# Kernel optimization log

Hardware: AMD Instinct MI355X
Metric: run time of the kernel (lower is better)

The kernel has to match this reference:

```python
import jax, jax.numpy as jnp
import numpy as np

N = 100000      # nodes
E = 1250000     # edges
DIN = 128       # in_channels
H = 64          # hidden
DOUT = 40       # out_channels


def setup_inputs() -> dict:
    key = jax.random.key(0)
    k0, k1, k2, k3 = jax.random.split(key, 4)
    x = jax.random.normal(k0, (N, DIN), dtype=jnp.float32)
    edge_index = jax.random.randint(k1, (2, E), 0, N, dtype=jnp.int32)
    # glorot-style init for the GCNConv linear layers
    W1 = jax.random.normal(k2, (DIN, H), dtype=jnp.float32) * np.float32(1.0 / np.sqrt(DIN))
    b1 = jnp.zeros((H,), dtype=jnp.float32)
    W2 = jax.random.normal(k3, (H, DOUT), dtype=jnp.float32) * np.float32(1.0 / np.sqrt(H))
    b2 = jnp.zeros((DOUT,), dtype=jnp.float32)
    return {"x": x, "W1": W1, "b1": b1, "W2": W2, "b2": b2, "edge_index": edge_index}


def reference(x, W1, b1, W2, b2, edge_index):
    # GCN normalization with added self-loops (PyG GCNConv default):
    # norm_e = deg(dst)^-1/2 * deg(src)^-1/2
    loop = jnp.arange(N, dtype=edge_index.dtype)
    src = jnp.concatenate([edge_index[0], loop])
    dst = jnp.concatenate([edge_index[1], loop])
    deg = jax.ops.segment_sum(jnp.ones(src.shape[0], x.dtype), dst, num_segments=N)
    dinv = jax.lax.rsqrt(deg)  # deg >= 1 thanks to self-loops
    norm = dinv[src] * dinv[dst]  # [E+N]

    def gcn_conv(h, W, b):
        h = h @ W                                     # [N, d_out] linear (no bias)
        msg = h[src] * norm[:, None]                  # gather + normalize
        return jax.ops.segment_sum(msg, dst, num_segments=N) + b  # scatter-add + bias

    h = jax.nn.relu(gcn_conv(x, W1, b1))  # dropout p=0.0 -> identity
    return gcn_conv(h, W2, b2)
```

## Files before the change

### kernel.cpp

```cpp
#include <hip/hip_runtime.h>
#include <hip/hip_fp16.h>

#define NN   100000
#define EE   1250000
#define DIN  128
#define HID  64
#define DOUT 40

#define BN   512
#define NB   196
#define CH   4096
#define SEG  8192
#define S_BLKS 306
#define G_BLKS 1563

typedef _Float16 v8h __attribute__((ext_vector_type(8)));
typedef float    v4f __attribute__((ext_vector_type(4)));

__device__ __forceinline__ void acc8(const float4& v, float4& lo, float4& hi) {
    const __half2* hp = (const __half2*)&v;
    float2 f0 = __half22float2(hp[0]), f1 = __half22float2(hp[1]);
    float2 f2 = __half22float2(hp[2]), f3 = __half22float2(hp[3]);
    lo.x += f0.x; lo.y += f0.y; lo.z += f1.x; lo.w += f1.y;
    hi.x += f2.x; hi.y += f2.y; hi.z += f3.x; hi.w += f3.y;
}

__global__ __launch_bounds__(256) void k_wprep(const float* __restrict__ W1,
                                               const float* __restrict__ W2,
                                               __half* __restrict__ w1frag,
                                               __half* __restrict__ w2frag,
                                               int* __restrict__ bucket_fill) {
    int t = threadIdx.x;
    if (blockIdx.x == 5 && t < NB) bucket_fill[t] = 0;
    int e = blockIdx.x * 256 + t;
    if (e < 1024) {
        int ct = e >> 8, ki = (e >> 6) & 3, l = e & 63;
        int q = l >> 4, n = l & 15;
        v8h o;
        #pragma unroll
        for (int j = 0; j < 8; ++j)
            o[j] = (_Float16)W1[(ki * 32 + q * 8 + j) * 64 + ct * 16 + n];
        ((v8h*)w1frag)[e] = o;
    } else {
        int e2 = e - 1024;
        if (e2 < 384) {
            int ct = e2 >> 7, ki = (e2 >> 6) & 1, l = e2 & 63;
            int q = l >> 4, n = l & 15;
            int col = ct * 16 + n;
            v8h o;
            #pragma unroll
            for (int j = 0; j < 8; ++j)
                o[j] = (col < DOUT) ? (_Float16)W2[(ki * 32 + q * 8 + j) * DOUT + col]
                                    : (_Float16)0.0f;
            ((v8h*)w2frag)[e2] = o;
        }
    }
}

__global__ __launch_bounds__(256) void k_fat(const int* __restrict__ src,
                                             const int* __restrict__ dst,
                                             int* __restrict__ bucket_fill,
                                             int* __restrict__ ebuf,
                                             const float* __restrict__ x,
                                             const __half* __restrict__ w1frag,
                                             __half* __restrict__ xw1h) {
    __shared__ int smem[4096];
    int t = threadIdx.x;
    if (blockIdx.x < S_BLKS) {
        int* hist  = smem;
        int* gbase = smem + 256;
        int* rcur  = smem + 512;
        for (int i = t; i < NB; i += 256) { hist[i] = 0; rcur[i] = 0; }
        __syncthreads();
        int e0 = blockIdx.x * CH;
        int ep[16], eb[16];
        #pragma unroll
        for (int j = 0; j < 16; ++j) {
            int e = e0 + j * 256 + t;
            bool valid = (e < EE);
            if (valid) {
                int dd_ = dst[e];
                ep[j] = (src[e] << 9) | (dd_ & 511);
                eb[j] = dd_ >> 9;
                atomicAdd(&hist[eb[j]], 1);
            } else {
                ep[j] = 0; eb[j] = -1;
            }
        }
        __syncthreads();
        for (int i = t; i < NB; i += 256)
            gbase[i] = atomicAdd(&bucket_fill[i], hist[i]);
        __syncthreads();
        #pragma unroll
        for (int j = 0; j < 16; ++j) {
            if (eb[j] >= 0) {
                int r = atomicAdd(&rcur[eb[j]], 1);
                ebuf[eb[j] * SEG + gbase[eb[j]] + r] = ep[j];
            }
        }
    } else {
        float4* sb4 = (float4*)smem;
        const float4* wf = (const float4*)w1frag;
        #pragma unroll
        for (int i = 0; i < 4; ++i) sb4[t + i * 256] = wf[t + i * 256];
        __syncthreads();
        const v8h* sbh = (const v8h*)sb4;
        int wv = t >> 6, l = t & 63;
        int q = l >> 4, n = l & 15;
        int row0 = (blockIdx.x - S_BLKS) * 64 + wv * 16;
        int m = row0 + n;
        bool mv = (m < NN);
        const float* xr = x + (size_t)(mv ? m : 0) * DIN + q * 8;
        v8h afrag[4];
        #pragma unroll
        for (int ki = 0; ki < 4; ++ki) {
            float4 u0 = mv ? ((const float4*)(xr + ki * 32))[0] : make_float4(0.f,0.f,0.f,0.f);
            float4 u1 = mv ? ((const float4*)(xr + ki * 32))[1] : make_float4(0.f,0.f,0.f,0.f);
            v8h a;
            a[0] = (_Float16)u0.x; a[1] = (_Float16)u0.y;
            a[2] = (_Float16)u0.z; a[3] = (_Float16)u0.w;
            a[4] = (_Float16)u1.x; a[5] = (_Float16)u1.y;
            a[6] = (_Float16)u1.z; a[7] = (_Float16)u1.w;
            afrag[ki] = a;
        }
        v4f acc[4];
        #pragma unroll
        for (int ct = 0; ct < 4; ++ct) acc[ct] = (v4f){0.f, 0.f, 0.f, 0.f};
        #pragma unroll
        for (int ct = 0; ct < 4; ++ct) {
            #pragma unroll
            for (int ki = 0; ki < 4; ++ki)
                acc[ct] = __builtin_amdgcn_mfma_f32_16x16x32_f16(
                    afrag[ki], sbh[(ct * 4 + ki) * 64 + l], acc[ct], 0, 0, 0);
        }
        _Float16* outh = (_Float16*)xw1h;
        #pragma unroll
        for (int r = 0; r < 4; ++r) {
            int rr = row0 + q * 4 + r;
            if (rr < NN) {
                #pragma unroll
                for (int ct = 0; ct < 4; ++ct)
                    outh[(size_t)rr * HID + ct * 16 + n] = (_Float16)acc[ct][r];
            }
        }
    }
}

__global__ __launch_bounds__(256) void kB_csr(const int* __restrict__ ebuf,
                                              const int* __restrict__ bucket_fill,
                                              int* __restrict__ pofs,
                                              float* __restrict__ dinv,
                                              int* __restrict__ esrc,
                                              __half* __restrict__ xw1h) {
    __shared__ int lcnt[BN], sA[BN], sB[BN], lcur[BN];
    int t = threadIdx.x;
    int b = blockIdx.x;
    int eb0 = b * SEG;
    int ecnt = bucket_fill[b];
    lcnt[t] = 0; lcnt[t + 256] = 0;
    __syncthreads();
    for (int j = t; j < ecnt; j += 256)
        atomicAdd(&lcnt[ebuf[eb0 + j] & 511], 1);
    __syncthreads();
    sA[t] = lcnt[t]; sA[t + 256] = lcnt[t + 256];
    __syncthreads();
    int* s = sA; int* d = sB;
    for (int off = 1; off < BN; off <<= 1) {
        d[t] = s[t] + ((t >= off) ? s[t - off] : 0);
        int i2 = t + 256;
        d[i2] = s[i2] + ((i2 >= off) ? s[i2 - off] : 0);
        __syncthreads();
        int* tmp = s; s = d; d = tmp;
    }
    int base_node = b * BN;
    #pragma unroll
    for (int k = 0; k < 2; ++k) {
        int i = t + k * 256;
        int excl = s[i] - lcnt[i];
        lcur[i] = excl;
        int node = base_node + i;
        if (node < NN) {
            pofs[node] = ((eb0 + excl) << 10) | lcnt[i];
            dinv[node] = rsqrtf((float)lcnt[i] + 1.0f);
        }
    }
    __syncthreads();
    for (int j = t; j < ecnt; j += 256) {
        int p = ebuf[eb0 + j];
        int r = atomicAdd(&lcur[p & 511], 1);
        esrc[eb0 + r] = p >> 9;
    }
    float4* xr4 = (float4*)xw1h;
    for (int i = t; i < BN * 8; i += 256) {
        int li = i >> 3;
        int node = base_node + li;
        if (node < NN) {
            float di = rsqrtf((float)lcnt[li] + 1.0f);
            float4 v = xr4[(size_t)node * 8 + (i & 7)];
            __half2* h = (__half2*)&v;
            #pragma unroll
            for (int u = 0; u < 4; ++u) {
                float2 f = __half22float2(h[u]);
                h[u] = __floats2half2_rn(f.x * di, f.y * di);
            }
            xr4[(size_t)node * 8 + (i & 7)] = v;
        }
    }
}

__global__ __launch_bounds__(256) void k_fuse(const __half* __restrict__ xw1h,
                                              const float* __restrict__ dinv,
                                              const int* __restrict__ pofs,
                                              const int* __restrict__ esrc,
                                              const float* __restrict__ b1,
                                              const __half* __restrict__ w2frag,
                                              __half* __restrict__ hw2p) {
    __shared__ float4 sb4[384];
    __shared__ __half sh[64 * 72];
    __shared__ float sb1[64];
    int t = threadIdx.x;
    const float4* wf = (const float4*)w2frag;
    if (t < 192) { sb4[t] = wf[t]; sb4[t + 192] = wf[t + 192]; }
    if (t >= 192) sb1[t - 192] = b1[t - 192];
    int d0 = blockIdx.x * 64;
    int g = t >> 3, q = t & 7;
    const float4* tab4 = (const float4*)xw1h;
    #pragma unroll
    for (int sub = 0; sub < 2; ++sub) {
        int d = d0 + g * 2 + sub;
        if (d < NN) {
            float4 lo = make_float4(0.f, 0.f, 0.f, 0.f);
            float4 hi = make_float4(0.f, 0.f, 0.f, 0.f);
            acc8(tab4[(size_t)d * 8 + q], lo, hi);
            int p = pofs[d];
            int j = p >> 10, je = j + (p & 1023);
            for (; j + 7 < je; j += 8) {
                int ss[8];
                #pragma unroll
                for (int u = 0; u < 8; ++u) ss[u] = esrc[j + u];
                float4 vv[8];
                #pragma unroll
                for (int u = 0; u < 8; ++u) vv[u] = tab4[(size_t)ss[u] * 8 + q];
                #pragma unroll
                for (int u = 0; u < 8; ++u) acc8(vv[u], lo, hi);
            }
            for (; j + 3 < je; j += 4) {
                float4 v0 = tab4[(size_t)esrc[j] * 8 + q];
                float4 v1 = tab4[(size_t)esrc[j + 1] * 8 + q];
                float4 v2 = tab4[(size_t)esrc[j + 2] * 8 + q];
                float4 v3 = tab4[(size_t)esrc[j + 3] * 8 + q];
                acc8(v0, lo, hi); acc8(v1, lo, hi);
                acc8(v2, lo, hi); acc8(v3, lo, hi);
            }
            for (; j < je; ++j)
                acc8(tab4[(size_t)esrc[j] * 8 + q], lo, hi);
            float dd = dinv[d];
            float4 st;
            __half2* hp = (__half2*)&st;
            hp[0] = __floats2half2_rn(dd * lo.x, dd * lo.y);
            hp[1] = __floats2half2_rn(dd * lo.z, dd * lo.w);
            hp[2] = __floats2half2_rn(dd * hi.x, dd * hi.y);
            hp[3] = __floats2half2_rn(dd * hi.z, dd * hi.w);
            *(float4*)(sh + (g * 2 + sub) * 72 + q * 8) = st;
        }
    }
    __syncthreads();
    const v8h* sbh = (const v8h*)sb4;
    int wv = t >> 6, l = t & 63;
    int qq = l >> 4, n = l & 15;
    int srow = wv * 16 + n;
    v8h afrag[2];
    #pragma unroll
    for (int ki = 0; ki < 2; ++ki) {
        v8h a = *(const v8h*)(sh + srow * 72 + ki * 32 + qq * 8);
        #pragma unroll
        for (int j = 0; j < 8; ++j) {
            float av = (float)a[j] + sb1[ki * 32 + qq * 8 + j];
            a[j] = (_Float16)fmaxf(av, 0.f);
        }
        afrag[ki] = a;
    }
    v4f acc[3];
    #pragma unroll
    for (int ct = 0; ct < 3; ++ct) acc[ct] = (v4f){0.f, 0.f, 0.f, 0.f};
    #pragma unroll
    for (int ct = 0; ct < 3; ++ct) {
        #pragma unroll
        for (int ki = 0; ki < 2; ++ki)
            acc[ct] = __builtin_amdgcn_mfma_f32_16x16x32_f16(
                afrag[ki], sbh[(ct * 2 + ki) * 64 + l], acc[ct], 0, 0, 0);
    }
    _Float16* outh = (_Float16*)hw2p;
    #pragma unroll
    for (int r = 0; r < 4; ++r) {
        int rr = d0 + wv * 16 + qq * 4 + r;
        if (rr < NN) {
            float di = dinv[rr];
            #pragma unroll
            for (int ct = 0; ct < 3; ++ct)
                outh[(size_t)rr * 64 + ct * 16 + n] = (_Float16)(acc[ct][r] * di);
        }
    }
}

__global__ __launch_bounds__(256) void k_agg2(const __half* __restrict__ hw2p,
                                              const float* __restrict__ dinv,
                                              const int* __restrict__ pofs,
                                              const int* __restrict__ esrc,
                                              const float* __restrict__ b2,
                                              float* __restrict__ out) {
    int t = threadIdx.x;
    int g = t >> 3, q = t & 7;
    int d = blockIdx.x * 32 + g;
    if (d >= NN) return;
    const float4* tab4 = (const float4*)hw2p;
    float4 lo = make_float4(0.f, 0.f, 0.f, 0.f);
    float4 hi = make_float4(0.f, 0.f, 0.f, 0.f);
    acc8(tab4[(size_t)d * 8 + q], lo, hi);
    int p = pofs[d];
    int j = p >> 10, je = j + (p & 1023);
    for (; j + 7 < je; j += 8) {
        int ss[8];
        #pragma unroll
        for (int u = 0; u < 8; ++u) ss[u] = esrc[j + u];
        float4 vv[8];
        #pragma unroll
        for (int u = 0; u < 8; ++u) vv[u] = tab4[(size_t)ss[u] * 8 + q];
        #pragma unroll
        for (int u = 0; u < 8; ++u) acc8(vv[u], lo, hi);
    }
    for (; j + 3 < je; j += 4) {
        float4 v0 = tab4[(size_t)esrc[j] * 8 + q];
        float4 v1 = tab4[(size_t)esrc[j + 1] * 8 + q];
        float4 v2 = tab4[(size_t)esrc[j + 2] * 8 + q];
        float4 v3 = tab4[(size_t)esrc[j + 3] * 8 + q];
        acc8(v0, lo, hi); acc8(v1, lo, hi);
        acc8(v2, lo, hi); acc8(v3, lo, hi);
    }
    for (; j < je; ++j)
        acc8(tab4[(size_t)esrc[j] * 8 + q], lo, hi);
    if (q < 5) {
        float dd = dinv[d];
        const float4* b24 = (const float4*)(b2 + q * 8);
        float4 bl = b24[0], bh = b24[1];
        float* op = out + (size_t)d * DOUT + q * 8;
        ((float4*)op)[0] = make_float4(dd * lo.x + bl.x, dd * lo.y + bl.y,
                                       dd * lo.z + bl.z, dd * lo.w + bl.w);
        ((float4*)op)[1] = make_float4(dd * hi.x + bh.x, dd * hi.y + bh.y,
                                       dd * hi.z + bh.z, dd * hi.w + bh.w);
    }
}

extern "C" void kernel_launch(void* const* d_in, const int* in_sizes, int n_in,
                              void* d_out, int out_size, void* d_ws, size_t ws_size,
                              hipStream_t stream) {
    const float* x  = (const float*)d_in[0];
    const float* W1 = (const float*)d_in[1];
    const float* b1 = (const float*)d_in[2];
    const float* W2 = (const float*)d_in[3];
    const float* b2 = (const float*)d_in[4];
    const int*   ei = (const int*)d_in[5];
    const int* src = ei;
    const int* dst = ei + EE;
    float* out = (float*)d_out;

    float* ws = (float*)d_ws;
    int*    bucket_fill = (int*)ws;
    int*    pofs        = (int*)ws + 256;
    float*  dinv        = ws + 100352;
    int*    ebuf        = (int*)ws + 200704;
    int*    esrc        = (int*)ws + 1806336;
    __half* xw1h        = (__half*)(ws + 3411968);
    __half* hw2p        = (__half*)(ws + 6611968);
    __half* w1frag      = (__half*)(ws + 9811968);
    __half* w2frag      = (__half*)(ws + 9816064);

    k_wprep <<<6, 256, 0, stream>>>(W1, W2, w1frag, w2frag, bucket_fill);
    k_fat   <<<S_BLKS + G_BLKS, 256, 0, stream>>>(src, dst, bucket_fill, ebuf, x, w1frag, xw1h);
    kB_csr  <<<NB, 256, 0, stream>>>(ebuf, bucket_fill, pofs, dinv, esrc, xw1h);
    k_fuse  <<<(NN + 63) / 64, 256, 0, stream>>>(xw1h, dinv, pofs, esrc, b1, w2frag, hw2p);
    k_agg2  <<<(NN + 31) / 32, 256, 0, stream>>>(hw2p, dinv, pofs, esrc, b2, out);
}
```

Baseline: 201.0 us.

## Switch gathers to edge-balanced chunks with shared-memory segmented atomic accumulation

Both aggregation kernels now split the CSR edge range of each 64-node tile evenly across 32 thread groups instead of giving one group per destination node. Each group keeps running sums and flushes them with shared-memory atomics when the destination changes. To support this, the local destination index is packed into the upper bits of esrc. The aim is to remove load imbalance from varying degrees and the tail loops, at the cost of LDS atomics, an extra barrier, and in agg2 idle lanes for q>=5 during the gather.

```diff
diff --git a/kernel.cpp b/kernel.cpp
--- a/kernel.cpp
+++ b/kernel.cpp
@@ -24,6 +24,21 @@
     lo.x += f0.x; lo.y += f0.y; lo.z += f1.x; lo.w += f1.y;
     hi.x += f2.x; hi.y += f2.y; hi.z += f3.x; hi.w += f3.y;
 }
+
+__device__ __forceinline__ void flush8(float* p, const float4& lo, const float4& hi) {
+    atomicAdd(p + 0, lo.x); atomicAdd(p + 1, lo.y);
+    atomicAdd(p + 2, lo.z); atomicAdd(p + 3, lo.w);
+    atomicAdd(p + 4, hi.x); atomicAdd(p + 5, hi.y);
+    atomicAdd(p + 6, hi.z); atomicAdd(p + 7, hi.w);
+}
+
+#define PROC(dl_, v_) { int dl__ = (dl_);                                        \
+    if (dl__ != cur) {                                                           \
+        if (cur >= 0) flush8(&lacc[(cur - dlo) * 72 + q * 8], lo, hi);           \
+        cur = dl__;                                                              \
+        lo = make_float4(0.f,0.f,0.f,0.f); hi = make_float4(0.f,0.f,0.f,0.f);    \
+    }                                                                            \
+    acc8(v_, lo, hi); }
 
 __global__ __launch_bounds__(256) void k_wprep(const float* __restrict__ W1,
                                                const float* __restrict__ W2,
@@ -188,7 +203,7 @@
     for (int j = t; j < ecnt; j += 256) {
         int p = ebuf[eb0 + j];
         int r = atomicAdd(&lcur[p & 511], 1);
-        esrc[eb0 + r] = p >> 9;
+        esrc[eb0 + r] = (p >> 9) | ((p & 511) << 17);
     }
     float4* xr4 = (float4*)xw1h;
     for (int i = t; i < BN * 8; i += 256) {
@@ -215,68 +230,73 @@
                                               const float* __restrict__ b1,
                                               const __half* __restrict__ w2frag,
                                               __half* __restrict__ hw2p) {
+    __shared__ float lacc[64 * 72];
     __shared__ float4 sb4[384];
-    __shared__ __half sh[64 * 72];
     __shared__ float sb1[64];
     int t = threadIdx.x;
     const float4* wf = (const float4*)w2frag;
     if (t < 192) { sb4[t] = wf[t]; sb4[t + 192] = wf[t + 192]; }
     if (t >= 192) sb1[t - 192] = b1[t - 192];
+    for (int i = t; i < 64 * 72; i += 256) lacc[i] = 0.f;
+    __syncthreads();
+
     int d0 = blockIdx.x * 64;
+    int dlo = d0 & 511;
+    int lastd = min(d0 + 63, NN - 1);
+    int pA = pofs[d0], pB = pofs[lastd];
+    int j0 = pA >> 10;
+    int j1 = (pB >> 10) + (pB & 1023);
     int g = t >> 3, q = t & 7;
+    int nchunk = (j1 - j0 + 31) >> 5;
+    int js = j0 + g * nchunk;
+    int je = min(js + nchunk, j1);
     const float4* tab4 = (const float4*)xw1h;
-    #pragma unroll
-    for (int sub = 0; sub < 2; ++sub) {
-        int d = d0 + g * 2 + sub;
-        if (d < NN) {
-            float4 lo = make_float4(0.f, 0.f, 0.f, 0.f);
-            float4 hi = make_float4(0.f, 0.f, 0.f, 0.f);
-            acc8(tab4[(size_t)d * 8 + q], lo, hi);
-            int p = pofs[d];
-            int j = p >> 10, je = j + (p & 1023);
-            for (; j + 7 < je; j += 8) {
-                int ss[8];
-                #pragma unroll
-                for (int u = 0; u < 8; ++u) ss[u] = esrc[j + u];
-                float4 vv[8];
-                #pragma unroll
-                for (int u = 0; u < 8; ++u) vv[u] = tab4[(size_t)ss[u] * 8 + q];
-                #pragma unroll
-                for (int u = 0; u < 8; ++u) acc8(vv[u], lo, hi);
-            }
-            for (; j + 3 < je; j += 4) {
-                float4 v0 = tab4[(size_t)esrc[j] * 8 + q];
-                float4 v1 = tab4[(size_t)esrc[j + 1] * 8 + q];
-                float4 v2 = tab4[(size_t)esrc[j + 2] * 8 + q];
-                float4 v3 = tab4[(size_t)esrc[j + 3] * 8 + q];
-                acc8(v0, lo, hi); acc8(v1, lo, hi);
-                acc8(v2, lo, hi); acc8(v3, lo, hi);
-            }
-            for (; j < je; ++j)
-                acc8(tab4[(size_t)esrc[j] * 8 + q], lo, hi);
-            float dd = dinv[d];
-            float4 st;
-            __half2* hp = (__half2*)&st;
-            hp[0] = __floats2half2_rn(dd * lo.x, dd * lo.y);
-            hp[1] = __floats2half2_rn(dd * lo.z, dd * lo.w);
-            hp[2] = __floats2half2_rn(dd * hi.x, dd * hi.y);
-            hp[3] = __floats2half2_rn(dd * hi.z, dd * hi.w);
-            *(float4*)(sh + (g * 2 + sub) * 72 + q * 8) = st;
-        }
-    }
-    __syncthreads();
+
+    float4 lo = make_float4(0.f,0.f,0.f,0.f), hi = make_float4(0.f,0.f,0.f,0.f);
+    int cur = -1;
+    int j = js;
+    for (; j + 3 < je; j += 4) {
+        int e0 = esrc[j], e1 = esrc[j+1], e2 = esrc[j+2], e3 = esrc[j+3];
+        float4 v0 = tab4[(size_t)(e0 & 0x1FFFF) * 8 + q];
+        float4 v1 = tab4[(size_t)(e1 & 0x1FFFF) * 8 + q];
+        float4 v2 = tab4[(size_t)(e2 & 0x1FFFF) * 8 + q];
+        float4 v3 = tab4[(size_t)(e3 & 0x1FFFF) * 8 + q];
+        PROC(e0 >> 17, v0); PROC(e1 >> 17, v1);
+        PROC(e2 >> 17, v2); PROC(e3 >> 17, v3);
+    }
+    for (; j < je; ++j) {
+        int e = esrc[j];
+        float4 v = tab4[(size_t)(e & 0x1FFFF) * 8 + q];
+        PROC(e >> 17, v);
+    }
+    if (cur >= 0) flush8(&lacc[(cur - dlo) * 72 + q * 8], lo, hi);
+    __syncthreads();
+
     const v8h* sbh = (const v8h*)sb4;
     int wv = t >> 6, l = t & 63;
     int qq = l >> 4, n = l & 15;
     int srow = wv * 16 + n;
+    int node = d0 + srow;
+    bool nv = (node < NN);
+    float dd = nv ? dinv[node] : 0.f;
     v8h afrag[2];
     #pragma unroll
     for (int ki = 0; ki < 2; ++ki) {
-        v8h a = *(const v8h*)(sh + srow * 72 + ki * 32 + qq * 8);
-        #pragma unroll
-        for (int j = 0; j < 8; ++j) {
-            float av = (float)a[j] + sb1[ki * 32 + qq * 8 + j];
-            a[j] = (_Float16)fmaxf(av, 0.f);
+        int ch = ki * 32 + qq * 8;
+        float4 f0 = *(const float4*)&lacc[srow * 72 + ch];
+        float4 f1 = *(const float4*)&lacc[srow * 72 + ch + 4];
+        v8h sf;
+        if (nv) sf = *(const v8h*)(xw1h + (size_t)node * HID + ch);
+        else {
+            #pragma unroll
+            for (int jj = 0; jj < 8; ++jj) sf[jj] = (_Float16)0.f;
+        }
+        float fa[8] = {f0.x, f0.y, f0.z, f0.w, f1.x, f1.y, f1.z, f1.w};
+        v8h a;
+        #pragma unroll
+        for (int jj = 0; jj < 8; ++jj) {
+            float av = (fa[jj] + (float)sf[jj]) * dd + sb1[ch + jj];
+            a[jj] = (_Float16)fmaxf(av, 0.f);
         }
         afrag[ki] = a;
     }
@@ -309,45 +329,62 @@
                                               const int* __restrict__ esrc,
                                               const float* __restrict__ b2,
                                               float* __restrict__ out) {
+    __shared__ float lacc[64 * 72];
     int t = threadIdx.x;
+    for (int i = t; i < 64 * 72; i += 256) lacc[i] = 0.f;
+    __syncthreads();
+
+    int d0 = blockIdx.x * 64;
+    int dlo = d0 & 511;
+    int lastd = min(d0 + 63, NN - 1);
+    int pA = pofs[d0], pB = pofs[lastd];
+    int j0 = pA >> 10;
+    int j1 = (pB >> 10) + (pB & 1023);
     int g = t >> 3, q = t & 7;
-    int d = blockIdx.x * 32 + g;
-    if (d >= NN) return;
     const float4* tab4 = (const float4*)hw2p;
-    float4 lo = make_float4(0.f, 0.f, 0.f, 0.f);
-    float4 hi = make_float4(0.f, 0.f, 0.f, 0.f);
-    acc8(tab4[(size_t)d * 8 + q], lo, hi);
-    int p = pofs[d];
-    int j = p >> 10, je = j + (p & 1023);
-    for (; j + 7 < je; j += 8) {
-        int ss[8];
-        #pragma unroll
-        for (int u = 0; u < 8; ++u) ss[u] = esrc[j + u];
-        float4 vv[8];
-        #pragma unroll
-        for (int u = 0; u < 8; ++u) vv[u] = tab4[(size_t)ss[u] * 8 + q];
-        #pragma unroll
-        for (int u = 0; u < 8; ++u) acc8(vv[u], lo, hi);
-    }
-    for (; j + 3 < je; j += 4) {
-        float4 v0 = tab4[(size_t)esrc[j] * 8 + q];
-        float4 v1 = tab4[(size_t)esrc[j + 1] * 8 + q];
-        float4 v2 = tab4[(size_t)esrc[j + 2] * 8 + q];
-        float4 v3 = tab4[(size_t)esrc[j + 3] * 8 + q];
-        acc8(v0, lo, hi); acc8(v1, lo, hi);
-        acc8(v2, lo, hi); acc8(v3, lo, hi);
-    }
-    for (; j < je; ++j)
-        acc8(tab4[(size_t)esrc[j] * 8 + q], lo, hi);
+
     if (q < 5) {
-        float dd = dinv[d];
-        const float4* b24 = (const float4*)(b2 + q * 8);
-        float4 bl = b24[0], bh = b24[1];
-        float* op = out + (size_t)d * DOUT + q * 8;
-        ((float4*)op)[0] = make_float4(dd * lo.x + bl.x, dd * lo.y + bl.y,
-                                       dd * lo.z + bl.z, dd * lo.w + bl.w);
-        ((float4*)op)[1] = make_float4(dd * hi.x + bh.x, dd * hi.y + bh.y,
-                                       dd * hi.z + bh.z, dd * hi.w + bh.w);
+        int nchunk = (j1 - j0 + 31) >> 5;
+        int js = j0 + g * nchunk;
+        int je = min(js + nchunk, j1);
+        float4 lo = make_float4(0.f,0.f,0.f,0.f), hi = make_float4(0.f,0.f,0.f,0.f);
+        int cur = -1;
+        int j = js;
+        for (; j + 3 < je; j += 4) {
+            int e0 = esrc[j], e1 = esrc[j+1], e2 = esrc[j+2], e3 = esrc[j+3];
+            float4 v0 = tab4[(size_t)(e0 & 0x1FFFF) * 8 + q];
+            float4 v1 = tab4[(size_t)(e1 & 0x1FFFF) * 8 + q];
+            float4 v2 = tab4[(size_t)(e2 & 0x1FFFF) * 8 + q];
+            float4 v3 = tab4[(size_t)(e3 & 0x1FFFF) * 8 + q];
+            PROC(e0 >> 17, v0); PROC(e1 >> 17, v1);
+            PROC(e2 >> 17, v2); PROC(e3 >> 17, v3);
+        }
+        for (; j < je; ++j) {
+            int e = esrc[j];
+            float4 v = tab4[(size_t)(e & 0x1FFFF) * 8 + q];
+            PROC(e >> 17, v);
+        }
+        if (cur >= 0) flush8(&lacc[(cur - dlo) * 72 + q * 8], lo, hi);
+    }
+    __syncthreads();
+
+    #pragma unroll
+    for (int sub = 0; sub < 2; ++sub) {
+        int ld = g * 2 + sub;
+        int d = d0 + ld;
+        if (d < NN && q < 5) {
+            float4 lo = *(const float4*)&lacc[ld * 72 + q * 8];
+            float4 hi = *(const float4*)&lacc[ld * 72 + q * 8 + 4];
+            acc8(tab4[(size_t)d * 8 + q], lo, hi);
+            float dd = dinv[d];
+            const float4* b24 = (const float4*)(b2 + q * 8);
+            float4 bl = b24[0], bh = b24[1];
+            float* op = out + (size_t)d * DOUT + q * 8;
+            ((float4*)op)[0] = make_float4(dd * lo.x + bl.x, dd * lo.y + bl.y,
+                                           dd * lo.z + bl.z, dd * lo.w + bl.w);
+            ((float4*)op)[1] = make_float4(dd * hi.x + bh.x, dd * hi.y + bh.y,
+                                           dd * hi.z + bh.z, dd * hi.w + bh.w);
+        }
     }
 }
 
@@ -379,5 +416,5 @@
     k_fat   <<<S_BLKS + G_BLKS, 256, 0, stream>>>(src, dst, bucket_fill, ebuf, x, w1frag, xw1h);
     kB_csr  <<<NB, 256, 0, stream>>>(ebuf, bucket_fill, pofs, dinv, esrc, xw1h);
     k_fuse  <<<(NN + 63) / 64, 256, 0, stream>>>(xw1h, dinv, pofs, esrc, b1, w2frag, hw2p);
-    k_agg2  <<<(NN + 31) / 32, 256, 0, stream>>>(hw2p, dinv, pofs, esrc, b2, out);
-}
+    k_agg2  <<<(NN + 63) / 64, 256, 0, stream>>>(hw2p, dinv, pofs, esrc, b2, out);
+}
```

New measurement: 242.4 us. 20.6% more time.

## Merge neighbor-pair edge loops using parity-tagged source indices in CSR

Applied to the files above, without the earlier changes.

The CSR build now packs the destination's local index into the high bits of each esrc entry. The fused and second aggregation kernels then process two consecutive destination nodes in one merged edge loop. Each edge is added to a running total, and the second node's share is selected by an FMA with the parity bit; the first node's result is recovered by subtraction. This is meant to cut loop-tail divergence and to balance degree variation across the two nodes. The cost is extra FMA work per edge and reliance on node ids fitting in 17 bits. k_agg2 now launches half as many blocks, each covering 64 nodes.

```diff
diff --git a/kernel.cpp b/kernel.cpp
--- a/kernel.cpp
+++ b/kernel.cpp
@@ -23,6 +23,24 @@
     float2 f2 = __half22float2(hp[2]), f3 = __half22float2(hp[3]);
     lo.x += f0.x; lo.y += f0.y; lo.z += f1.x; lo.w += f1.y;
     hi.x += f2.x; hi.y += f2.y; hi.z += f3.x; hi.w += f3.y;
+}
+
+__device__ __forceinline__ void fma8(const float4& v, float s, float4& lo, float4& hi) {
+    const __half2* hp = (const __half2*)&v;
+    float2 f0 = __half22float2(hp[0]), f1 = __half22float2(hp[1]);
+    float2 f2 = __half22float2(hp[2]), f3 = __half22float2(hp[3]);
+    lo.x += f0.x * s; lo.y += f0.y * s; lo.z += f1.x * s; lo.w += f1.y * s;
+    hi.x += f2.x * s; hi.y += f2.y * s; hi.z += f3.x * s; hi.w += f3.y * s;
+}
+
+__device__ __forceinline__ void sthalf8(__half* p, const float4& lo, const float4& hi, float d) {
+    float4 st;
+    __half2* hp = (__half2*)&st;
+    hp[0] = __floats2half2_rn(lo.x * d, lo.y * d);
+    hp[1] = __floats2half2_rn(lo.z * d, lo.w * d);
+    hp[2] = __floats2half2_rn(hi.x * d, hi.y * d);
+    hp[3] = __floats2half2_rn(hi.z * d, hi.w * d);
+    *(float4*)p = st;
 }
 
 __global__ __launch_bounds__(256) void k_wprep(const float* __restrict__ W1,
@@ -188,7 +206,7 @@
     for (int j = t; j < ecnt; j += 256) {
         int p = ebuf[eb0 + j];
         int r = atomicAdd(&lcur[p & 511], 1);
-        esrc[eb0 + r] = p >> 9;
+        esrc[eb0 + r] = (p >> 9) | ((p & 511) << 17);
     }
     float4* xr4 = (float4*)xw1h;
     for (int i = t; i < BN * 8; i += 256) {
@@ -215,56 +233,65 @@
                                               const float* __restrict__ b1,
                                               const __half* __restrict__ w2frag,
                                               __half* __restrict__ hw2p) {
+    __shared__ __half sh[64 * 72];
     __shared__ float4 sb4[384];
-    __shared__ __half sh[64 * 72];
     __shared__ float sb1[64];
     int t = threadIdx.x;
     const float4* wf = (const float4*)w2frag;
     if (t < 192) { sb4[t] = wf[t]; sb4[t + 192] = wf[t + 192]; }
     if (t >= 192) sb1[t - 192] = b1[t - 192];
+
     int d0 = blockIdx.x * 64;
     int g = t >> 3, q = t & 7;
+    int dA = d0 + 2 * g;
     const float4* tab4 = (const float4*)xw1h;
-    #pragma unroll
-    for (int sub = 0; sub < 2; ++sub) {
-        int d = d0 + g * 2 + sub;
-        if (d < NN) {
-            float4 lo = make_float4(0.f, 0.f, 0.f, 0.f);
-            float4 hi = make_float4(0.f, 0.f, 0.f, 0.f);
-            acc8(tab4[(size_t)d * 8 + q], lo, hi);
-            int p = pofs[d];
-            int j = p >> 10, je = j + (p & 1023);
-            for (; j + 7 < je; j += 8) {
-                int ss[8];
-                #pragma unroll
-                for (int u = 0; u < 8; ++u) ss[u] = esrc[j + u];
-                float4 vv[8];
-                #pragma unroll
-                for (int u = 0; u < 8; ++u) vv[u] = tab4[(size_t)ss[u] * 8 + q];
-                #pragma unroll
-                for (int u = 0; u < 8; ++u) acc8(vv[u], lo, hi);
-            }
-            for (; j + 3 < je; j += 4) {
-                float4 v0 = tab4[(size_t)esrc[j] * 8 + q];
-                float4 v1 = tab4[(size_t)esrc[j + 1] * 8 + q];
-                float4 v2 = tab4[(size_t)esrc[j + 2] * 8 + q];
-                float4 v3 = tab4[(size_t)esrc[j + 3] * 8 + q];
-                acc8(v0, lo, hi); acc8(v1, lo, hi);
-                acc8(v2, lo, hi); acc8(v3, lo, hi);
-            }
-            for (; j < je; ++j)
-                acc8(tab4[(size_t)esrc[j] * 8 + q], lo, hi);
-            float dd = dinv[d];
-            float4 st;
-            __half2* hp = (__half2*)&st;
-            hp[0] = __floats2half2_rn(dd * lo.x, dd * lo.y);
-            hp[1] = __floats2half2_rn(dd * lo.z, dd * lo.w);
-            hp[2] = __floats2half2_rn(dd * hi.x, dd * hi.y);
-            hp[3] = __floats2half2_rn(dd * hi.z, dd * hi.w);
-            *(float4*)(sh + (g * 2 + sub) * 72 + q * 8) = st;
-        }
+    float4 tl = make_float4(0.f,0.f,0.f,0.f), th = make_float4(0.f,0.f,0.f,0.f);
+    float4 bl = make_float4(0.f,0.f,0.f,0.f), bh = make_float4(0.f,0.f,0.f,0.f);
+    int j = 0, je = 0;
+    if (dA < NN) {
+        int pA_ = pofs[dA], pB_ = pofs[dA + 1];
+        j  = pA_ >> 10;
+        je = (pB_ >> 10) + (pB_ & 1023);
+        float4 sA = tab4[(size_t)dA * 8 + q];
+        float4 sB = tab4[(size_t)(dA + 1) * 8 + q];
+        acc8(sA, tl, th);
+        acc8(sB, tl, th);
+        acc8(sB, bl, bh);
+    }
+    for (; j + 7 < je; j += 8) {
+        int e[8];
+        #pragma unroll
+        for (int u = 0; u < 8; ++u) e[u] = esrc[j + u];
+        float4 v[8];
+        #pragma unroll
+        for (int u = 0; u < 8; ++u) v[u] = tab4[(size_t)(e[u] & 0x1FFFF) * 8 + q];
+        #pragma unroll
+        for (int u = 0; u < 8; ++u) {
+            float s = (float)((e[u] >> 17) & 1);
+            acc8(v[u], tl, th);
+            fma8(v[u], s, bl, bh);
+        }
+    }
+    for (; j < je; ++j) {
+        int e = esrc[j];
+        float4 v = tab4[(size_t)(e & 0x1FFFF) * 8 + q];
+        float s = (float)((e >> 17) & 1);
+        acc8(v, tl, th);
+        fma8(v, s, bl, bh);
+    }
+    if (dA < NN) {
+        float diA = dinv[dA], diB = dinv[dA + 1];
+        float4 al = make_float4(tl.x - bl.x, tl.y - bl.y, tl.z - bl.z, tl.w - bl.w);
+        float4 ah = make_float4(th.x - bh.x, th.y - bh.y, th.z - bh.z, th.w - bh.w);
+        sthalf8(sh + (2 * g) * 72 + q * 8, al, ah, diA);
+        sthalf8(sh + (2 * g + 1) * 72 + q * 8, bl, bh, diB);
+    } else {
+        float4 z = make_float4(0.f,0.f,0.f,0.f);
+        sthalf8(sh + (2 * g) * 72 + q * 8, z, z, 0.f);
+        sthalf8(sh + (2 * g + 1) * 72 + q * 8, z, z, 0.f);
     }
     __syncthreads();
+
     const v8h* sbh = (const v8h*)sb4;
     int wv = t >> 6, l = t & 63;
     int qq = l >> 4, n = l & 15;
@@ -274,9 +301,9 @@
     for (int ki = 0; ki < 2; ++ki) {
         v8h a = *(const v8h*)(sh + srow * 72 + ki * 32 + qq * 8);
         #pragma unroll
-        for (int j = 0; j < 8; ++j) {
-            float av = (float)a[j] + sb1[ki * 32 + qq * 8 + j];
-            a[j] = (_Float16)fmaxf(av, 0.f);
+        for (int jj = 0; jj < 8; ++jj) {
+            float av = (float)a[jj] + sb1[ki * 32 + qq * 8 + jj];
+            a[jj] = (_Float16)fmaxf(av, 0.f);
         }
         afrag[ki] = a;
     }
@@ -311,43 +338,55 @@
                                               float* __restrict__ out) {
     int t = threadIdx.x;
     int g = t >> 3, q = t & 7;
-    int d = blockIdx.x * 32 + g;
-    if (d >= NN) return;
+    int d0 = blockIdx.x * 64;
+    int dA = d0 + 2 * g;
+    if (dA >= NN) return;
     const float4* tab4 = (const float4*)hw2p;
-    float4 lo = make_float4(0.f, 0.f, 0.f, 0.f);
-    float4 hi = make_float4(0.f, 0.f, 0.f, 0.f);
-    acc8(tab4[(size_t)d * 8 + q], lo, hi);
-    int p = pofs[d];
-    int j = p >> 10, je = j + (p & 1023);
+    float4 tl = make_float4(0.f,0.f,0.f,0.f), th = make_float4(0.f,0.f,0.f,0.f);
+    float4 bl = make_float4(0.f,0.f,0.f,0.f), bh = make_float4(0.f,0.f,0.f,0.f);
+    int pA_ = pofs[dA], pB_ = pofs[dA + 1];
+    int j  = pA_ >> 10;
+    int je = (pB_ >> 10) + (pB_ & 1023);
+    float4 sA = tab4[(size_t)dA * 8 + q];
+    float4 sB = tab4[(size_t)(dA + 1) * 8 + q];
+    acc8(sA, tl, th);
+    acc8(sB, tl, th);
+    acc8(sB, bl, bh);
     for (; j + 7 < je; j += 8) {
-        int ss[8];
-        #pragma unroll
-        for (int u = 0; u < 8; ++u) ss[u] = esrc[j + u];
-        float4 vv[8];
-        #pragma unroll
-        for (int u = 0; u < 8; ++u) vv[u] = tab4[(size_t)ss[u] * 8 + q];
-        #pragma unroll
-        for (int u = 0; u < 8; ++u) acc8(vv[u], lo, hi);
-    }
-    for (; j + 3 < je; j += 4) {
-        float4 v0 = tab4[(size_t)esrc[j] * 8 + q];
-        float4 v1 = tab4[(size_t)esrc[j + 1] * 8 + q];
-        float4 v2 = tab4[(size_t)esrc[j + 2] * 8 + q];
-        float4 v3 = tab4[(size_t)esrc[j + 3] * 8 + q];
-        acc8(v0, lo, hi); acc8(v1, lo, hi);
-        acc8(v2, lo, hi); acc8(v3, lo, hi);
-    }
-    for (; j < je; ++j)
-        acc8(tab4[(size_t)esrc[j] * 8 + q], lo, hi);
+        int e[8];
+        #pragma unroll
+        for (int u = 0; u < 8; ++u) e[u] = esrc[j + u];
+        float4 v[8];
+        #pragma unroll
+        for (int u = 0; u < 8; ++u) v[u] = tab4[(size_t)(e[u] & 0x1FFFF) * 8 + q];
+        #pragma unroll
+        for (int u = 0; u < 8; ++u) {
+            float s = (float)((e[u] >> 17) & 1);
+            acc8(v[u], tl, th);
+            fma8(v[u], s, bl, bh);
+        }
+    }
+    for (; j < je; ++j) {
+        int e = esrc[j];
+        float4 v = tab4[(size_t)(e & 0x1FFFF) * 8 + q];
+        float s = (float)((e >> 17) & 1);
+        acc8(v, tl, th);
+        fma8(v, s, bl, bh);
+    }
     if (q < 5) {
-        float dd = dinv[d];
+        float diA = dinv[dA], diB = dinv[dA + 1];
         const float4* b24 = (const float4*)(b2 + q * 8);
-        float4 bl = b24[0], bh = b24[1];
-        float* op = out + (size_t)d * DOUT + q * 8;
-        ((float4*)op)[0] = make_float4(dd * lo.x + bl.x, dd * lo.y + bl.y,
-                                       dd * lo.z + bl.z, dd * lo.w + bl.w);
-        ((float4*)op)[1] = make_float4(dd * hi.x + bh.x, dd * hi.y + bh.y,
-                                       dd * hi.z + bh.z, dd * hi.w + bh.w);
+        float4 c0 = b24[0], c1 = b24[1];
+        float* opA = out + (size_t)dA * DOUT + q * 8;
+        ((float4*)opA)[0] = make_float4((tl.x - bl.x) * diA + c0.x, (tl.y - bl.y) * diA + c0.y,
+                                        (tl.z - bl.z) * diA + c0.z, (tl.w - bl.w) * diA + c0.w);
+        ((float4*)opA)[1] = make_float4((th.x - bh.x) * diA + c1.x, (th.y - bh.y) * diA + c1.y,
+                                        (th.z - bh.z) * diA + c1.z, (th.w - bh.w) * diA + c1.w);
+        float* opB = out + (size_t)(dA + 1) * DOUT + q * 8;
+        ((float4*)opB)[0] = make_float4(bl.x * diB + c0.x, bl.y * diB + c0.y,
+                                        bl.z * diB + c0.z, bl.w * diB + c0.w);
+        ((float4*)opB)[1] = make_float4(bh.x * diB + c1.x, bh.y * diB + c1.y,
+                                        bh.z * diB + c1.z, bh.w * diB + c1.w);
     }
 }
 
@@ -379,5 +418,5 @@
     k_fat   <<<S_BLKS + G_BLKS, 256, 0, stream>>>(src, dst, bucket_fill, ebuf, x, w1frag, xw1h);
     kB_csr  <<<NB, 256, 0, stream>>>(ebuf, bucket_fill, pofs, dinv, esrc, xw1h);
     k_fuse  <<<(NN + 63) / 64, 256, 0, stream>>>(xw1h, dinv, pofs, esrc, b1, w2frag, hw2p);
-    k_agg2  <<<(NN + 31) / 32, 256, 0, stream>>>(hw2p, dinv, pofs, esrc, b2, out);
-}
+    k_agg2  <<<(NN + 63) / 64, 256, 0, stream>>>(hw2p, dinv, pofs, esrc, b2, out);
+}
```

Measured after the change: 202.8 us. Within noise of the previous version (+0.9%).
